# Optimization experiments

Measured on AMD Instinct MI355X. Metric: run time of the kernel, lower is better.

## Reference

```python
import jax, jax.numpy as jnp
import numpy as np

IN_SHAPE, OUT_SHAPE = 64, 256  # FoldingBlock(64, 256, ...)
REPEAT = OUT_SHAPE // IN_SHAPE  # 4


def sample_2d(m, n):
    # Reproduces SANet.points + SANet.sample_2D exactly (numpy constants).
    xs = np.linspace(-0.3, 0.3, 46)
    ys = np.linspace(-0.3, 0.3, 46)
    X, Y = np.meshgrid(xs, ys)            # (46,46) each, 'xy' indexing
    pts = np.stack([X, Y])                # (2,46,46)
    ix = np.round(np.linspace(0, 45, m)).astype(int)
    iy = np.round(np.linspace(0, 45, n)).astype(int)
    gx, gy = np.meshgrid(ix, iy)          # (n,m)
    p = pts[:, gx.ravel(), gy.ravel()].T  # (m*n, 2)
    return jnp.asarray(p, dtype=jnp.float32)


def _lin_relu(x, W, b):
    return jax.nn.relu(x @ W + b)


def setup_inputs() -> dict:
    key = jax.random.key(0)
    ks = jax.random.split(key, 16)
    s = 0.02  # small init scale keeps softmax logits well-conditioned
    d = {
        "p": jax.random.normal(ks[0], (128, 64, 512), dtype=jnp.float32),
        # upmlp1: MLP([514, 512]) (shared by both up() calls)
        "W_up": jax.random.normal(ks[1], (514, 512), dtype=jnp.float32) * s,
        "b_up": jnp.zeros((512,), jnp.float32),
        # self_attn1: M_h = MLP([1024,256])
        "Wh": jax.random.normal(ks[2], (1024, 256), dtype=jnp.float32) * s,
        "bh": jnp.zeros((256,), jnp.float32),
        # M_l = MLP([1024,256])
        "Wl": jax.random.normal(ks[3], (1024, 256), dtype=jnp.float32) * s,
        "bl": jnp.zeros((256,), jnp.float32),
        # M_g = MLP([1024,1024])
        "Wg": jax.random.normal(ks[4], (1024, 1024), dtype=jnp.float32) * s,
        "bg": jnp.zeros((1024,), jnp.float32),
        # M_f = MLP([1024,512,256]) -> two Linear+ReLU layers
        "Wf1": jax.random.normal(ks[5], (1024, 512), dtype=jnp.float32) * s,
        "bf1": jnp.zeros((512,), jnp.float32),
        "Wf2": jax.random.normal(ks[6], (512, 256), dtype=jnp.float32) * s,
        "bf2": jnp.zeros((256,), jnp.float32),
        # M_down: MLP([1024, 512])
        "W_down": jax.random.normal(ks[7], (1024, 512), dtype=jnp.float32) * s,
        "b_down": jnp.zeros((512,), jnp.float32),
        "m": 16,
        "n": 16,
    }
    return d


def _up(p, pts, W_up, b_up, Wh, bh, Wl, bl, Wg, bg, Wf1, bf1, Wf2, bf2):
    # p: (B, 64, 512) -> (B, 256, 512) via torch-style repeat (tile)
    B = p.shape[0]
    p = jnp.tile(p, (1, REPEAT, 1))
    p2d = jnp.concatenate([p, jnp.broadcast_to(pts[None], (B,) + pts.shape)], -1)  # (B,256,514)
    p2d = _lin_relu(p2d, W_up, b_up)                  # (B,256,512)
    p = jnp.concatenate([p, p2d], -1)                  # (B,256,1024)
    # SelfAttention (hand-rolled: separate projections + softmax + bmm)
    h = _lin_relu(p, Wh, bh)                           # (B,256,256)
    l = _lin_relu(p, Wl, bl)                           # (B,256,256)
    g = _lin_relu(p, Wg, bg)                           # (B,256,1024)
    mm = jnp.einsum("bmc,bnc->bmn", l, h)             # l @ h^T
    attn = jax.nn.softmax(mm, axis=-1)
    applied = jnp.einsum("bmn,bnc->bmc", attn, g)      # (B,256,1024)
    x = p + applied
    # M_f = MLP([1024,512,256]): ReLU after every Linear
    return _lin_relu(_lin_relu(x, Wf1, bf1), Wf2, bf2)  # (B,256,256)


def _down(p, W_down, b_down):
    # (B,256,256) -> (B,64,1024) -> MLP([1024,512])
    B = p.shape[0]
    p = p.reshape(B, IN_SHAPE, REPEAT * p.shape[2])
    return _lin_relu(p, W_down, b_down)                # (B,64,512)


def reference(p, W_up, b_up, Wh, bh, Wl, bl, Wg, bg, Wf1, bf1, Wf2, bf2,
              W_down, b_down, m, n):
    pts = sample_2d(int(m), int(n))                    # (m*n, 2) constant grid
    attn_params = (Wh, bh, Wl, bl, Wg, bg, Wf1, bf1, Wf2, bf2)
    p1 = _up(p, pts, W_up, b_up, *attn_params)         # (B,256,256)
    p2 = _down(p1, W_down, b_down)                     # (B,64,512)
    p_delta = p - p2
    p2u = _up(p_delta, pts, W_up, b_up, *attn_params)  # shared weights with first up
    return p1 + p2u                                    # (B,256,256)
```

## Files before the change

kernel.cpp:

```cpp
#include <hip/hip_runtime.h>
#include <cstdint>
#include <cstddef>


typedef unsigned short u16;
typedef __bf16 bf16x8 __attribute__((ext_vector_type(8)));
typedef float f32x4 __attribute__((ext_vector_type(4)));

__device__ __forceinline__ u16 f2bf(float f) {
    unsigned u = __builtin_bit_cast(unsigned, f);
    unsigned r = (u + 0x7fffu + ((u >> 16) & 1u)) >> 16;
    return (u16)r;
}
__device__ __forceinline__ float bf2f(u16 h) {
    unsigned u = ((unsigned)h) << 16;
    return __builtin_bit_cast(float, u);
}
__device__ __forceinline__ bf16x8 ldfrag(const u16* p) {
    return __builtin_bit_cast(bf16x8, *reinterpret_cast<const uint4*>(p));
}
__device__ __forceinline__ void gload16(const u16* g, u16* l) {
    __builtin_amdgcn_global_load_lds((__attribute__((address_space(1))) void*)g,
                                     (__attribute__((address_space(3))) void*)l,
                                     16, 0, 0);
}

#define FENCE asm volatile("" ::: "memory")
#define BAR() do { FENCE; __builtin_amdgcn_s_barrier(); FENCE; } while (0)

template<int MODE>
__global__ __launch_bounds__(512, 1)
void bp(const u16* __restrict__ A0, const u16* __restrict__ A1,
        const u16* __restrict__ Bt, const float* __restrict__ bias,
        const float* __restrict__ EXf, const u16* __restrict__ EXb,
        u16* __restrict__ outB, u16* __restrict__ out1, u16* __restrict__ out2,
        int K, long sB)
{
    __shared__ __align__(16) u16 As[2][16384];
    __shared__ __align__(16) u16 Bs[2][16384];

    const int b    = blockIdx.y;
    const int tid  = threadIdx.x;
    const int lane = tid & 63;
    const int w    = tid >> 6;
    const int wr   = w >> 2, wc = w & 3;
    const int wrow0 = wr * 128, wcol0 = wc * 64;
    const int gn0  = blockIdx.x * 256;
    const int lm   = lane & 15, hk = lane >> 4;
    const int NT   = K / 64;

    const int srow = tid & 255;
    const int su   = tid >> 8;

    const u16* gA0;
    const u16* gA1 = nullptr;
    if constexpr (MODE == 0) {
        gA0 = A0 + ((size_t)b << 15) + (size_t)(srow & 63) * 512 + su * 8;
    } else if constexpr (MODE == 1) {
        gA0 = A0 + ((size_t)b << 15) + (size_t)(srow & 63) * 512 + su * 8;
        gA1 = A1 + ((size_t)b << 17) + (size_t)srow * 512 + su * 8;
    } else if constexpr (MODE == 3) {
        gA0 = A0 + ((size_t)b << 16) + (size_t)srow * 256 + su * 8;
    } else {
        gA0 = A0 + ((size_t)b << 18) + (size_t)srow * 1024 + su * 8;
    }
    const u16* gB0 = Bt + (size_t)b * sB + (size_t)(gn0 + srow) * K + su * 8;

    u16* dA = &As[0][(size_t)(su * 256 + srow) * 8];
    u16* dB = &Bs[0][(size_t)(su * 256 + srow) * 8];

    auto stgA = [&](int kt, int buf, int rp) {
        const u16* g;
        if constexpr (MODE == 1) g = (kt < 8) ? (gA0 + kt * 64) : (gA1 + (kt - 8) * 64);
        else                     g = gA0 + kt * 64;
        u16* d = dA + buf * 16384 + rp * 8192;
        gload16(g + rp * 32,      d);
        gload16(g + rp * 32 + 16, d + 4096);
    };
    auto stgB = [&](int kt, int buf, int rp) {
        const u16* g = gB0 + kt * 64 + rp * 32;
        u16* d = dB + buf * 16384 + rp * 8192;
        gload16(g,      d);
        gload16(g + 16, d + 4096);
    };

    const u16* rA = &As[0][(size_t)(hk * 256 + wrow0 + lm) * 8];
    const u16* rB = &Bs[0][(size_t)(hk * 256 + wcol0 + lm) * 8];

    f32x4 acc[8][4];
    #pragma unroll
    for (int i = 0; i < 8; ++i)
        #pragma unroll
        for (int j = 0; j < 4; ++j)
            acc[i][j] = (f32x4){0.f, 0.f, 0.f, 0.f};

    stgA(0, 0, 0); stgA(0, 0, 1);
    stgB(0, 0, 0); stgB(0, 0, 1);
    stgA(1, 1, 0); stgB(1, 1, 0);
    asm volatile("s_waitcnt vmcnt(4)" ::: "memory");
    BAR();

    for (int t = 0; t < NT; ++t) {
        const int buf = t & 1, nx = buf ^ 1;
        const u16* a  = rA + buf * 16384;
        const u16* bb = rB + buf * 16384;
        bf16x8 aq[4], bq[4];

        #pragma unroll
        for (int i = 0; i < 4; ++i) aq[i] = ldfrag(a + i * 128);
        #pragma unroll
        for (int j = 0; j < 4; ++j) bq[j] = ldfrag(bb + j * 128);
        if (t + 1 < NT) stgA(t + 1, nx, 1);
        BAR();
        __builtin_amdgcn_s_setprio(1);
        #pragma unroll
        for (int i = 0; i < 4; ++i)
            #pragma unroll
            for (int j = 0; j < 4; ++j)
                acc[i][j] = __builtin_amdgcn_mfma_f32_16x16x32_bf16(aq[i], bq[j], acc[i][j], 0, 0, 0);
        __builtin_amdgcn_s_setprio(0);
        BAR();

        #pragma unroll
        for (int i = 0; i < 4; ++i) aq[i] = ldfrag(a + (4 + i) * 128);
        if (t + 1 < NT) stgB(t + 1, nx, 1);
        BAR();
        __builtin_amdgcn_s_setprio(1);
        #pragma unroll
        for (int i = 0; i < 4; ++i)
            #pragma unroll
            for (int j = 0; j < 4; ++j)
                acc[4 + i][j] = __builtin_amdgcn_mfma_f32_16x16x32_bf16(aq[i], bq[j], acc[4 + i][j], 0, 0, 0);
        __builtin_amdgcn_s_setprio(0);
        BAR();

        #pragma unroll
        for (int i = 0; i < 4; ++i) aq[i] = ldfrag(a + 8192 + i * 128);
        #pragma unroll
        for (int j = 0; j < 4; ++j) bq[j] = ldfrag(bb + 8192 + j * 128);
        if (t + 2 < NT) stgA(t + 2, buf, 0);
        BAR();
        __builtin_amdgcn_s_setprio(1);
        #pragma unroll
        for (int i = 0; i < 4; ++i)
            #pragma unroll
            for (int j = 0; j < 4; ++j)
                acc[i][j] = __builtin_amdgcn_mfma_f32_16x16x32_bf16(aq[i], bq[j], acc[i][j], 0, 0, 0);
        __builtin_amdgcn_s_setprio(0);
        BAR();

        #pragma unroll
        for (int i = 0; i < 4; ++i) aq[i] = ldfrag(a + 8192 + (4 + i) * 128);
        if (t + 2 < NT) stgB(t + 2, buf, 0);
        if (t + 2 < NT) { asm volatile("s_waitcnt vmcnt(4)" ::: "memory"); }
        else            { asm volatile("s_waitcnt vmcnt(0)" ::: "memory"); }
        BAR();
        __builtin_amdgcn_s_setprio(1);
        #pragma unroll
        for (int i = 0; i < 4; ++i)
            #pragma unroll
            for (int j = 0; j < 4; ++j)
                acc[4 + i][j] = __builtin_amdgcn_mfma_f32_16x16x32_bf16(aq[i], bq[j], acc[4 + i][j], 0, 0, 0);
        __builtin_amdgcn_s_setprio(0);
        BAR();
    }

    #pragma unroll
    for (int i = 0; i < 8; ++i) {
        const int rowb = wrow0 + i * 16 + hk * 4;
        #pragma unroll
        for (int j = 0; j < 4; ++j) {
            const int col = gn0 + wcol0 + j * 16 + lm;
            float v4[4];
            #pragma unroll
            for (int r = 0; r < 4; ++r) v4[r] = acc[i][j][r];

            if constexpr (MODE == 0) {
                #pragma unroll
                for (int r = 0; r < 4; ++r) {
                    const int row = rowb + r;
                    float v = v4[r];
                    const float px = -0.3f + 0.04f * (float)(row >> 4);
                    const float py = -0.3f + 0.04f * (float)(row & 15);
                    v += px * EXf[(size_t)512 * 512 + col] + py * EXf[(size_t)513 * 512 + col];
                    v = fmaxf(v + bias[col], 0.0f);
                    outB[((size_t)b << 17) + (size_t)row * 512 + col] = f2bf(v);
                }
            } else if constexpr (MODE == 1) {
                if (col < 512) {
                    #pragma unroll
                    for (int r = 0; r < 4; ++r) {
                        const int row = rowb + r;
                        float v = fmaxf(v4[r] + bias[col], 0.0f);
                        if (col < 256) outB[((size_t)b << 16) + (size_t)row * 256 + col] = f2bf(v);
                        else           out1[((size_t)b << 16) + (size_t)row * 256 + (col - 256)] = f2bf(v);
                    }
                } else {
                    ushort4 o;
                    o.x = f2bf(fmaxf(v4[0] + bias[col], 0.0f));
                    o.y = f2bf(fmaxf(v4[1] + bias[col], 0.0f));
                    o.z = f2bf(fmaxf(v4[2] + bias[col], 0.0f));
                    o.w = f2bf(fmaxf(v4[3] + bias[col], 0.0f));
                    *reinterpret_cast<ushort4*>(out2 + ((size_t)b << 18) +
                        (size_t)(col - 512) * 256 + rowb) = o;
                }
            } else if constexpr (MODE == 3) {
                #pragma unroll
                for (int r = 0; r < 4; ++r) {
                    const int row = rowb + r;
                    float v = v4[r];
                    float cv;
                    if (col < 512) {
                        const size_t ridx = ((size_t)b << 15) + (size_t)(row & 63) * 512 + col;
                        cv = EXf ? EXf[ridx] : bf2f(EXb[ridx]);
                    } else {
                        cv = bf2f(A1[((size_t)b << 17) + (size_t)row * 512 + (col - 512)]);
                    }
                    v += cv;
                    outB[((size_t)b << 18) + (size_t)row * 1024 + col] = f2bf(v);
                }
            } else {
                #pragma unroll
                for (int r = 0; r < 4; ++r) {
                    const int row = rowb + r;
                    float v = fmaxf(v4[r] + bias[col], 0.0f);
                    outB[((size_t)b << 17) + (size_t)row * 512 + col] = f2bf(v);
                }
            }
        }
    }
}

template<int MODE>
__global__ __launch_bounds__(256, 2)
void mg(const u16* __restrict__ A0, const u16* __restrict__ Bt,
        const float* __restrict__ bias, const float* __restrict__ EXf,
        float* __restrict__ outF, u16* __restrict__ outB,
        int K, long sB)
{
    constexpr int BK = 64;
    constexpr int UMASK = 7;

    __shared__ __align__(16) u16 As[2][128 * 64];
    __shared__ __align__(16) u16 Bs[2][128 * 64];

    const int b    = blockIdx.z;
    const int tid  = threadIdx.x;
    const int lane = tid & 63;
    const int w    = tid >> 6;
    const int wr   = w >> 1, wc = w & 1;
    const int wrow0 = wr * 64, wcol0 = wc * 64;
    const int gm0  = blockIdx.y * 128;
    const int gn0  = blockIdx.x * 128;
    const int lm   = lane & 15, hk = lane >> 4;
    const int NT = K / BK;

    auto stage = [&](int kt, int buf) {
        const int kb = kt * BK;
        #pragma unroll
        for (int t = 0; t < 4; ++t) {
            const int idx = tid + t * 256;
            const int row = idx >> 3, u = idx & UMASK;
            const int kk = kb + ((u ^ (row & UMASK)) << 3);
            const u16* ga;
            if constexpr (MODE == 2) {
                ga = A0 + ((size_t)b << 16) + (size_t)(gm0 + row) * 256 + kk;
            } else if constexpr (MODE == 5) {
                ga = A0 + ((size_t)b << 17) + (size_t)(gm0 + row) * 512 + kk;
            } else {
                int gr = gm0 + row; if (gr > 63) gr = 63;
                ga = A0 + ((size_t)b << 16) + (size_t)(gr * 4 + (kk >> 8)) * 256 + (kk & 255);
            }
            gload16(ga, &As[buf][(size_t)(w * 64 + t * 256) * 8]);
        }
        #pragma unroll
        for (int t = 0; t < 4; ++t) {
            const int idx = tid + t * 256;
            const int row = idx >> 3, u = idx & UMASK;
            const int kk = kb + ((u ^ (row & UMASK)) << 3);
            gload16(Bt + (size_t)b * sB + (size_t)(gn0 + row) * K + kk,
                    &Bs[buf][(size_t)(w * 64 + t * 256) * 8]);
        }
    };

    f32x4 acc[4][4];
    #pragma unroll
    for (int i = 0; i < 4; ++i)
        #pragma unroll
        for (int j = 0; j < 4; ++j)
            acc[i][j] = (f32x4){0.f, 0.f, 0.f, 0.f};

    stage(0, 0);
    if (NT > 1) stage(1, 1);

    for (int kt = 0; kt < NT; ++kt) {
        const int cur = kt & 1;
        if (kt == NT - 1) asm volatile("s_waitcnt vmcnt(0)" ::: "memory");
        else              asm volatile("s_waitcnt vmcnt(8)" ::: "memory");
        __builtin_amdgcn_s_barrier();
        FENCE;

        #pragma unroll
        for (int ks = 0; ks < 2; ++ks) {
            bf16x8 af[4], bfr[4];
            #pragma unroll
            for (int i = 0; i < 4; ++i) {
                const int row = wrow0 + i * 16 + lm;
                af[i] = ldfrag(&As[cur][(size_t)row * BK + (((ks * 4 + hk) ^ (row & UMASK)) << 3)]);
            }
            #pragma unroll
            for (int j = 0; j < 4; ++j) {
                const int row = wcol0 + j * 16 + lm;
                bfr[j] = ldfrag(&Bs[cur][(size_t)row * BK + (((ks * 4 + hk) ^ (row & UMASK)) << 3)]);
            }
            __builtin_amdgcn_s_setprio(1);
            #pragma unroll
            for (int i = 0; i < 4; ++i)
                #pragma unroll
                for (int j = 0; j < 4; ++j)
                    acc[i][j] = __builtin_amdgcn_mfma_f32_16x16x32_bf16(af[i], bfr[j], acc[i][j], 0, 0, 0);
            __builtin_amdgcn_s_setprio(0);
        }

        FENCE;
        __builtin_amdgcn_s_barrier();
        if (kt + 2 < NT) stage(kt + 2, cur);
    }

    #pragma unroll
    for (int i = 0; i < 4; ++i) {
        #pragma unroll
        for (int r = 0; r < 4; ++r) {
            const int row = gm0 + wrow0 + i * 16 + hk * 4 + r;
            if (MODE == 6 && row >= 64) continue;
            #pragma unroll
            for (int j = 0; j < 4; ++j) {
                const int col = gn0 + wcol0 + j * 16 + lm;
                float v = acc[i][j][r];
                if constexpr (MODE == 2) {
                    outF[((size_t)b << 16) + (size_t)row * 256 + col] = v;
                } else if constexpr (MODE == 5) {
                    v = fmaxf(v + bias[col], 0.0f);
                    const size_t oidx = ((size_t)b << 16) + (size_t)row * 256 + col;
                    if (EXf) v += EXf[oidx];
                    outF[oidx] = v;
                    if (outB) outB[oidx] = f2bf(v);
                } else {
                    v = fmaxf(v + bias[col], 0.0f);
                    const size_t oidx = ((size_t)b << 15) + (size_t)row * 512 + col;
                    v = EXf[oidx] - v;
                    outB[oidx] = f2bf(v);
                }
            }
        }
    }
}

template<bool F32IN>
__global__ __launch_bounds__(256)
void transpose_k(const void* __restrict__ in_, u16* __restrict__ out, int R, int C)
{
    __shared__ float t[64][65];
    const size_t zo = (size_t)blockIdx.z * (size_t)R * C;
    const int c0 = blockIdx.x * 64, r0 = blockIdx.y * 64;
    const int x = threadIdx.x, y = threadIdx.y;
    #pragma unroll
    for (int i = 0; i < 16; ++i) {
        const int r = y * 16 + i;
        float v;
        if constexpr (F32IN) v = ((const float*)in_)[zo + (size_t)(r0 + r) * C + c0 + x];
        else                 v = bf2f(((const u16*)in_)[zo + (size_t)(r0 + r) * C + c0 + x]);
        t[r][x] = v;
    }
    __syncthreads();
    #pragma unroll
    for (int i = 0; i < 16; ++i) {
        const int c = y * 16 + i;
        out[zo + (size_t)(c0 + c) * R + r0 + x] = f2bf(t[x][c]);
    }
}

__global__ __launch_bounds__(256)
void cvt_k(const float* __restrict__ in, u16* __restrict__ out, int n4)
{
    int i = blockIdx.x * 256 + threadIdx.x;
    const int stride = gridDim.x * 256;
    for (; i < n4; i += stride) {
        float4 v = ((const float4*)in)[i];
        ushort4 o;
        o.x = f2bf(v.x); o.y = f2bf(v.y); o.z = f2bf(v.z); o.w = f2bf(v.w);
        ((ushort4*)out)[i] = o;
    }
}

__global__ __launch_bounds__(512)
void concat3_k(const float* __restrict__ a, const float* __restrict__ bb,
               const float* __restrict__ c, float* __restrict__ o)
{
    const int i = blockIdx.x * 512 + threadIdx.x;
    if (i < 256)       o[i] = a[i];
    else if (i < 512)  o[i] = bb[i - 256];
    else if (i < 1536) o[i] = c[i - 512];
}

__global__ __launch_bounds__(64)
void softmax_k(const float* __restrict__ logits, u16* __restrict__ attn)
{
    const size_t row = blockIdx.x;
    const float4 v = ((const float4*)(logits + row * 256))[threadIdx.x];
    float mx = fmaxf(fmaxf(v.x, v.y), fmaxf(v.z, v.w));
    #pragma unroll
    for (int o = 32; o > 0; o >>= 1) mx = fmaxf(mx, __shfl_xor(mx, o));
    float e0 = expf(v.x - mx), e1 = expf(v.y - mx), e2 = expf(v.z - mx), e3 = expf(v.w - mx);
    float s = e0 + e1 + e2 + e3;
    #pragma unroll
    for (int o = 32; o > 0; o >>= 1) s += __shfl_xor(s, o);
    const float inv = 1.0f / s;
    ushort4 o;
    o.x = f2bf(e0 * inv); o.y = f2bf(e1 * inv); o.z = f2bf(e2 * inv); o.w = f2bf(e3 * inv);
    ((ushort4*)(attn + row * 256))[threadIdx.x] = o;
}

extern "C" void kernel_launch(void* const* d_in, const int* in_sizes, int n_in,
                              void* d_out, int out_size, void* d_ws, size_t ws_size,
                              hipStream_t stream)
{
    const float* p      = (const float*)d_in[0];
    const float* W_up   = (const float*)d_in[1];
    const float* b_up   = (const float*)d_in[2];
    const float* Wh     = (const float*)d_in[3];
    const float* bh     = (const float*)d_in[4];
    const float* Wl     = (const float*)d_in[5];
    const float* bl     = (const float*)d_in[6];
    const float* Wg     = (const float*)d_in[7];
    const float* bg_    = (const float*)d_in[8];
    const float* Wf1    = (const float*)d_in[9];
    const float* bf1    = (const float*)d_in[10];
    const float* Wf2    = (const float*)d_in[11];
    const float* bf2v   = (const float*)d_in[12];
    const float* W_down = (const float*)d_in[13];
    const float* b_down = (const float*)d_in[14];

    const int B = in_sizes[0] / 32768;
    float* out = (float*)d_out;

    char* wsp = (char*)d_ws;
    auto alloc = [&](size_t bytes) -> char* {
        char* r = wsp; wsp += (bytes + 255) & ~(size_t)255; return r;
    };

    u16* WupT  = (u16*)alloc((size_t)512 * 512 * 2);
    u16* WhlgT = (u16*)alloc((size_t)1536 * 1024 * 2);
    u16* Wf1T  = (u16*)alloc((size_t)512 * 1024 * 2);
    u16* Wf2T  = (u16*)alloc((size_t)256 * 512 * 2);
    u16* WdT   = (u16*)alloc((size_t)512 * 1024 * 2);
    float* bias_hlg = (float*)alloc((size_t)1536 * 4);
    u16* pbf   = (u16*)alloc((size_t)B * 32768 * 2);

    const size_t fixed_used = (size_t)(wsp - (char*)d_ws);
    const size_t perB = 1903104;
    int BC = B;
    while (BC > 1 && fixed_used + (size_t)BC * perB + 4096 > ws_size) BC >>= 1;

    u16* upout = (u16*)alloc((size_t)BC * 131072 * 2);
    u16* gT    = (u16*)alloc((size_t)BC * 262144 * 2);
    u16* xb    = (u16*)alloc((size_t)BC * 262144 * 2);
    u16* hb    = (u16*)alloc((size_t)BC * 65536 * 2);
    u16* lb    = (u16*)alloc((size_t)BC * 65536 * 2);
    u16* atb   = (u16*)alloc((size_t)BC * 65536 * 2);
    u16* p1bf  = (u16*)alloc((size_t)BC * 65536 * 2);
    u16* pdbf  = (u16*)alloc((size_t)BC * 32768 * 2);
    float* lgt = (float*)xb;

    const dim3 tb(64, 4);
    {
        int n4 = B * 8192;
        int nb = (n4 + 255) / 256; if (nb > 2048) nb = 2048;
        cvt_k<<<dim3(nb), dim3(256), 0, stream>>>(p, pbf, n4);
        transpose_k<true><<<dim3(8, 8, 1),  tb, 0, stream>>>(W_up, WupT, 512, 512);
        transpose_k<true><<<dim3(4, 16, 1), tb, 0, stream>>>(Wh, WhlgT, 1024, 256);
        transpose_k<true><<<dim3(4, 16, 1), tb, 0, stream>>>(Wl, WhlgT + (size_t)256 * 1024, 1024, 256);
        transpose_k<true><<<dim3(16, 16, 1),tb, 0, stream>>>(Wg, WhlgT + (size_t)512 * 1024, 1024, 1024);
        transpose_k<true><<<dim3(8, 16, 1), tb, 0, stream>>>(Wf1, Wf1T, 1024, 512);
        transpose_k<true><<<dim3(4, 8, 1),  tb, 0, stream>>>(Wf2, Wf2T, 512, 256);
        transpose_k<true><<<dim3(8, 16, 1), tb, 0, stream>>>(W_down, WdT, 1024, 512);
        concat3_k<<<dim3(3), dim3(512), 0, stream>>>(bh, bl, bg_, bias_hlg);
    }

    auto run_up = [&](const u16* pin_bf, const float* pin_f32, const u16* pin_ebf,
                      float* f2outF, u16* f2outB, const float* f2EXf, int bc) {
        bp<0><<<dim3(2, bc), dim3(512), 0, stream>>>(
            pin_bf, nullptr, WupT, b_up, W_up, nullptr, upout, nullptr, nullptr, 512, 0);
        bp<1><<<dim3(6, bc), dim3(512), 0, stream>>>(
            pin_bf, upout, WhlgT, bias_hlg, nullptr, nullptr, hb, lb, gT, 1024, 0);
        mg<2><<<dim3(2, 2, bc), dim3(256), 0, stream>>>(
            lb, hb, nullptr, nullptr, lgt, nullptr, 256, 65536);
        softmax_k<<<dim3(bc * 256), dim3(64), 0, stream>>>(lgt, atb);
        bp<3><<<dim3(4, bc), dim3(512), 0, stream>>>(
            atb, upout, gT, nullptr, pin_f32, pin_ebf, xb, nullptr, nullptr, 256, 262144);
        bp<4><<<dim3(2, bc), dim3(512), 0, stream>>>(
            xb, nullptr, Wf1T, bf1, nullptr, nullptr, upout, nullptr, nullptr, 1024, 0);
        mg<5><<<dim3(2, 2, bc), dim3(256), 0, stream>>>(
            upout, Wf2T, bf2v, f2EXf, f2outF, f2outB, 512, 0);
    };

    for (int b0 = 0; b0 < B; b0 += BC) {
        const int bc = (B - b0 < BC) ? (B - b0) : BC;
        const u16*   pin_bf  = pbf + (size_t)b0 * 32768;
        const float* pin_f32 = p   + (size_t)b0 * 32768;
        float* outc = out + (size_t)b0 * 65536;
        run_up(pin_bf, pin_f32, nullptr, outc, p1bf, nullptr, bc);
        mg<6><<<dim3(4, 1, bc), dim3(256), 0, stream>>>(
            p1bf, WdT, b_down, pin_f32, nullptr, pdbf, 1024, 0);
        run_up(pdbf, nullptr, pdbf, outc, nullptr, outc, bc);
    }
}
```

Measured before the change: 869.0 us.

## Use inline-asm LDS reads, unswizzled k-major smem layout, and split lgkm waits

Replaces the C++ LDS fragment loads with inline ds_read_b128 on precomputed LDS byte addresses, adding explicit lgkmcnt waits with sched barriers in both GEMM kernels. In the mg kernel the XOR-swizzled row-major LDS tile becomes a k-chunk-major layout, and all fragments for both k-substeps are issued up front so the second batch of reads overlaps the first batch of MFMAs. The aim is to cut address arithmetic and let LDS latency hide behind MFMA work. The risks are LDS bank conflicts from dropping the swizzle, and scheduling constraints from the inline asm that the compiler cannot reorder around.

```diff
diff --git a/kernel.cpp b/kernel.cpp
--- a/kernel.cpp
+++ b/kernel.cpp
@@ -16,17 +16,25 @@
     unsigned u = ((unsigned)h) << 16;
     return __builtin_bit_cast(float, u);
 }
-__device__ __forceinline__ bf16x8 ldfrag(const u16* p) {
-    return __builtin_bit_cast(bf16x8, *reinterpret_cast<const uint4*>(p));
-}
 __device__ __forceinline__ void gload16(const u16* g, u16* l) {
     __builtin_amdgcn_global_load_lds((__attribute__((address_space(1))) void*)g,
                                      (__attribute__((address_space(3))) void*)l,
                                      16, 0, 0);
 }
+__device__ __forceinline__ unsigned ldsaddr(const u16* p) {
+    return (unsigned)(size_t)(const __attribute__((address_space(3))) u16*)p;
+}
+__device__ __forceinline__ bf16x8 dsr128(unsigned a) {
+    f32x4 r;
+    asm volatile("ds_read_b128 %0, %1" : "=v"(r) : "v"(a));
+    return __builtin_bit_cast(bf16x8, r);
+}
 
 #define FENCE asm volatile("" ::: "memory")
 #define BAR() do { FENCE; __builtin_amdgcn_s_barrier(); FENCE; } while (0)
+#define VMC(N) asm volatile("s_waitcnt vmcnt(" #N ")" ::: "memory")
+#define LGKM(N) do { asm volatile("s_waitcnt lgkmcnt(" #N ")" ::: "memory"); \
+                     __builtin_amdgcn_sched_barrier(0); } while (0)
 
 template<int MODE>
 __global__ __launch_bounds__(512, 1)
@@ -84,8 +92,8 @@
         gload16(g + 16, d + 4096);
     };
 
-    const u16* rA = &As[0][(size_t)(hk * 256 + wrow0 + lm) * 8];
-    const u16* rB = &Bs[0][(size_t)(hk * 256 + wcol0 + lm) * 8];
+    const unsigned aBase = ldsaddr(&As[0][0]) + (unsigned)(hk * 256 + wrow0 + lm) * 16u;
+    const unsigned bBase = ldsaddr(&Bs[0][0]) + (unsigned)(hk * 256 + wcol0 + lm) * 16u;
 
     f32x4 acc[8][4];
     #pragma unroll
@@ -93,77 +101,72 @@
         #pragma unroll
         for (int j = 0; j < 4; ++j)
             acc[i][j] = (f32x4){0.f, 0.f, 0.f, 0.f};
+
+#define MFMA_Q(IB) do { \
+    _Pragma("unroll") for (int i_ = 0; i_ < 4; ++i_) \
+        _Pragma("unroll") for (int j_ = 0; j_ < 4; ++j_) \
+            acc[(IB) + i_][j_] = __builtin_amdgcn_mfma_f32_16x16x32_bf16( \
+                aq[i_], bq[j_], acc[(IB) + i_][j_], 0, 0, 0); \
+} while (0)
 
     stgA(0, 0, 0); stgA(0, 0, 1);
     stgB(0, 0, 0); stgB(0, 0, 1);
     stgA(1, 1, 0); stgB(1, 1, 0);
-    asm volatile("s_waitcnt vmcnt(4)" ::: "memory");
+    VMC(4);
     BAR();
 
     for (int t = 0; t < NT; ++t) {
         const int buf = t & 1, nx = buf ^ 1;
-        const u16* a  = rA + buf * 16384;
-        const u16* bb = rB + buf * 16384;
+        const unsigned ab = aBase + (unsigned)buf * 32768u;
+        const unsigned bb = bBase + (unsigned)buf * 32768u;
         bf16x8 aq[4], bq[4];
 
         #pragma unroll
-        for (int i = 0; i < 4; ++i) aq[i] = ldfrag(a + i * 128);
-        #pragma unroll
-        for (int j = 0; j < 4; ++j) bq[j] = ldfrag(bb + j * 128);
+        for (int i = 0; i < 4; ++i) aq[i] = dsr128(ab + (unsigned)(i * 256));
+        #pragma unroll
+        for (int j = 0; j < 4; ++j) bq[j] = dsr128(bb + (unsigned)(j * 256));
         if (t + 1 < NT) stgA(t + 1, nx, 1);
         BAR();
+        LGKM(0);
         __builtin_amdgcn_s_setprio(1);
-        #pragma unroll
-        for (int i = 0; i < 4; ++i)
-            #pragma unroll
-            for (int j = 0; j < 4; ++j)
-                acc[i][j] = __builtin_amdgcn_mfma_f32_16x16x32_bf16(aq[i], bq[j], acc[i][j], 0, 0, 0);
+        MFMA_Q(0);
         __builtin_amdgcn_s_setprio(0);
         BAR();
 
         #pragma unroll
-        for (int i = 0; i < 4; ++i) aq[i] = ldfrag(a + (4 + i) * 128);
+        for (int i = 0; i < 4; ++i) aq[i] = dsr128(ab + (unsigned)(1024 + i * 256));
         if (t + 1 < NT) stgB(t + 1, nx, 1);
         BAR();
+        LGKM(0);
         __builtin_amdgcn_s_setprio(1);
-        #pragma unroll
-        for (int i = 0; i < 4; ++i)
-            #pragma unroll
-            for (int j = 0; j < 4; ++j)
-                acc[4 + i][j] = __builtin_amdgcn_mfma_f32_16x16x32_bf16(aq[i], bq[j], acc[4 + i][j], 0, 0, 0);
+        MFMA_Q(4);
         __builtin_amdgcn_s_setprio(0);
         BAR();
 
         #pragma unroll
-        for (int i = 0; i < 4; ++i) aq[i] = ldfrag(a + 8192 + i * 128);
-        #pragma unroll
-        for (int j = 0; j < 4; ++j) bq[j] = ldfrag(bb + 8192 + j * 128);
+        for (int i = 0; i < 4; ++i) aq[i] = dsr128(ab + (unsigned)(16384 + i * 256));
+        #pragma unroll
+        for (int j = 0; j < 4; ++j) bq[j] = dsr128(bb + (unsigned)(16384 + j * 256));
         if (t + 2 < NT) stgA(t + 2, buf, 0);
         BAR();
+        LGKM(0);
         __builtin_amdgcn_s_setprio(1);
-        #pragma unroll
-        for (int i = 0; i < 4; ++i)
-            #pragma unroll
-            for (int j = 0; j < 4; ++j)
-                acc[i][j] = __builtin_amdgcn_mfma_f32_16x16x32_bf16(aq[i], bq[j], acc[i][j], 0, 0, 0);
+        MFMA_Q(0);
         __builtin_amdgcn_s_setprio(0);
         BAR();
 
         #pragma unroll
-        for (int i = 0; i < 4; ++i) aq[i] = ldfrag(a + 8192 + (4 + i) * 128);
+        for (int i = 0; i < 4; ++i) aq[i] = dsr128(ab + (unsigned)(17408 + i * 256));
         if (t + 2 < NT) stgB(t + 2, buf, 0);
-        if (t + 2 < NT) { asm volatile("s_waitcnt vmcnt(4)" ::: "memory"); }
-        else            { asm volatile("s_waitcnt vmcnt(0)" ::: "memory"); }
-        BAR();
+        if (t + 2 < NT) { VMC(4); } else { VMC(0); }
+        BAR();
+        LGKM(0);
         __builtin_amdgcn_s_setprio(1);
-        #pragma unroll
-        for (int i = 0; i < 4; ++i)
-            #pragma unroll
-            for (int j = 0; j < 4; ++j)
-                acc[4 + i][j] = __builtin_amdgcn_mfma_f32_16x16x32_bf16(aq[i], bq[j], acc[4 + i][j], 0, 0, 0);
+        MFMA_Q(4);
         __builtin_amdgcn_s_setprio(0);
         BAR();
     }
+#undef MFMA_Q
 
     #pragma unroll
     for (int i = 0; i < 8; ++i) {
@@ -238,9 +241,6 @@
         float* __restrict__ outF, u16* __restrict__ outB,
         int K, long sB)
 {
-    constexpr int BK = 64;
-    constexpr int UMASK = 7;
-
     __shared__ __align__(16) u16 As[2][128 * 64];
     __shared__ __align__(16) u16 Bs[2][128 * 64];
 
@@ -253,15 +253,15 @@
     const int gm0  = blockIdx.y * 128;
     const int gn0  = blockIdx.x * 128;
     const int lm   = lane & 15, hk = lane >> 4;
-    const int NT = K / BK;
+    const int NT = K / 64;
 
     auto stage = [&](int kt, int buf) {
-        const int kb = kt * BK;
-        #pragma unroll
-        for (int t = 0; t < 4; ++t) {
-            const int idx = tid + t * 256;
-            const int row = idx >> 3, u = idx & UMASK;
-            const int kk = kb + ((u ^ (row & UMASK)) << 3);
+        const int kb = kt * 64;
+        #pragma unroll
+        for (int tp = 0; tp < 4; ++tp) {
+            const int idx = tid + tp * 256;
+            const int U = idx >> 7, row = idx & 127;
+            const int kk = kb + U * 8;
             const u16* ga;
             if constexpr (MODE == 2) {
                 ga = A0 + ((size_t)b << 16) + (size_t)(gm0 + row) * 256 + kk;
@@ -271,18 +271,21 @@
                 int gr = gm0 + row; if (gr > 63) gr = 63;
                 ga = A0 + ((size_t)b << 16) + (size_t)(gr * 4 + (kk >> 8)) * 256 + (kk & 255);
             }
-            gload16(ga, &As[buf][(size_t)(w * 64 + t * 256) * 8]);
+            gload16(ga, &As[buf][(size_t)idx * 8]);
         }
         #pragma unroll
-        for (int t = 0; t < 4; ++t) {
-            const int idx = tid + t * 256;
-            const int row = idx >> 3, u = idx & UMASK;
-            const int kk = kb + ((u ^ (row & UMASK)) << 3);
+        for (int tp = 0; tp < 4; ++tp) {
+            const int idx = tid + tp * 256;
+            const int U = idx >> 7, row = idx & 127;
+            const int kk = kb + U * 8;
             gload16(Bt + (size_t)b * sB + (size_t)(gn0 + row) * K + kk,
-                    &Bs[buf][(size_t)(w * 64 + t * 256) * 8]);
+                    &Bs[buf][(size_t)idx * 8]);
         }
     };
 
+    const unsigned aBase = ldsaddr(&As[0][0]) + (unsigned)(hk * 128 + wrow0 + lm) * 16u;
+    const unsigned bBase = ldsaddr(&Bs[0][0]) + (unsigned)(hk * 128 + wcol0 + lm) * 16u;
+
     f32x4 acc[4][4];
     #pragma unroll
     for (int i = 0; i < 4; ++i)
@@ -295,33 +298,36 @@
 
     for (int kt = 0; kt < NT; ++kt) {
         const int cur = kt & 1;
-        if (kt == NT - 1) asm volatile("s_waitcnt vmcnt(0)" ::: "memory");
-        else              asm volatile("s_waitcnt vmcnt(8)" ::: "memory");
+        if (kt == NT - 1) { VMC(0); } else { VMC(8); }
         __builtin_amdgcn_s_barrier();
         FENCE;
-
-        #pragma unroll
-        for (int ks = 0; ks < 2; ++ks) {
-            bf16x8 af[4], bfr[4];
+        const unsigned ab = aBase + (unsigned)cur * 16384u;
+        const unsigned bb = bBase + (unsigned)cur * 16384u;
+        bf16x8 a0[4], b0[4], a1[4], b1[4];
+        #pragma unroll
+        for (int i = 0; i < 4; ++i) a0[i] = dsr128(ab + (unsigned)(i * 256));
+        #pragma unroll
+        for (int j = 0; j < 4; ++j) b0[j] = dsr128(bb + (unsigned)(j * 256));
+        #pragma unroll
+        for (int i = 0; i < 4; ++i) a1[i] = dsr128(ab + (unsigned)(8192 + i * 256));
+        #pragma unroll
+        for (int j = 0; j < 4; ++j) b1[j] = dsr128(bb + (unsigned)(8192 + j * 256));
+        LGKM(8);
+        __builtin_amdgcn_s_setprio(1);
+        #pragma unroll
+        for (int i = 0; i < 4; ++i)
             #pragma unroll
-            for (int i = 0; i < 4; ++i) {
-                const int row = wrow0 + i * 16 + lm;
-                af[i] = ldfrag(&As[cur][(size_t)row * BK + (((ks * 4 + hk) ^ (row & UMASK)) << 3)]);
-            }
+            for (int j = 0; j < 4; ++j)
+                acc[i][j] = __builtin_amdgcn_mfma_f32_16x16x32_bf16(a0[i], b0[j], acc[i][j], 0, 0, 0);
+        __builtin_amdgcn_s_setprio(0);
+        LGKM(0);
+        __builtin_amdgcn_s_setprio(1);
+        #pragma unroll
+        for (int i = 0; i < 4; ++i)
             #pragma unroll
-            for (int j = 0; j < 4; ++j) {
-                const int row = wcol0 + j * 16 + lm;
-                bfr[j] = ldfrag(&Bs[cur][(size_t)row * BK + (((ks * 4 + hk) ^ (row & UMASK)) << 3)]);
-            }
-            __builtin_amdgcn_s_setprio(1);
-            #pragma unroll
-            for (int i = 0; i < 4; ++i)
-                #pragma unroll
-                for (int j = 0; j < 4; ++j)
-                    acc[i][j] = __builtin_amdgcn_mfma_f32_16x16x32_bf16(af[i], bfr[j], acc[i][j], 0, 0, 0);
-            __builtin_amdgcn_s_setprio(0);
-        }
-
+            for (int j = 0; j < 4; ++j)
+                acc[i][j] = __builtin_amdgcn_mfma_f32_16x16x32_bf16(a1[i], b1[j], acc[i][j], 0, 0, 0);
+        __builtin_amdgcn_s_setprio(0);
         FENCE;
         __builtin_amdgcn_s_barrier();
         if (kt + 2 < NT) stage(kt + 2, cur);
```

After: 886.6 us. 1.02x slower.

## Dedupe repeated rows in up-projection GEMM and fuse logits with softmax

Applied to the files above, without the earlier changes.

The up-projection GEMM now multiplies only the 64 distinct input rows per batch, two batches per block, instead of the 256 repeated rows. Each result is expanded in the epilogue to the four repeated output rows, each with its own grid coordinate term, which cuts MFMA work for that stage to a quarter. The separate fp32 logits GEMM and softmax kernel are replaced by one kernel that computes l·h^T and does a row softmax in registers using a cross-wave LDS reduction, so the fp32 logits never go through global memory. The new up kernel launches bc/2 blocks in z, so an odd chunk size would drop a batch.

```diff
diff --git a/kernel.cpp b/kernel.cpp
--- a/kernel.cpp
+++ b/kernel.cpp
@@ -24,9 +24,20 @@
                                      (__attribute__((address_space(3))) void*)l,
                                      16, 0, 0);
 }
+__device__ __forceinline__ unsigned ldsaddr(const u16* p) {
+    return (unsigned)(size_t)(const __attribute__((address_space(3))) u16*)p;
+}
+__device__ __forceinline__ bf16x8 dsr128(unsigned a) {
+    f32x4 r;
+    asm volatile("ds_read_b128 %0, %1" : "=v"(r) : "v"(a));
+    return __builtin_bit_cast(bf16x8, r);
+}
 
 #define FENCE asm volatile("" ::: "memory")
 #define BAR() do { FENCE; __builtin_amdgcn_s_barrier(); FENCE; } while (0)
+#define VMC(N) asm volatile("s_waitcnt vmcnt(" #N ")" ::: "memory")
+#define LGKM(N) do { asm volatile("s_waitcnt lgkmcnt(" #N ")" ::: "memory"); \
+                     __builtin_amdgcn_sched_barrier(0); } while (0)
 
 template<int MODE>
 __global__ __launch_bounds__(512, 1)
@@ -54,9 +65,7 @@
 
     const u16* gA0;
     const u16* gA1 = nullptr;
-    if constexpr (MODE == 0) {
-        gA0 = A0 + ((size_t)b << 15) + (size_t)(srow & 63) * 512 + su * 8;
-    } else if constexpr (MODE == 1) {
+    if constexpr (MODE == 1) {
         gA0 = A0 + ((size_t)b << 15) + (size_t)(srow & 63) * 512 + su * 8;
         gA1 = A1 + ((size_t)b << 17) + (size_t)srow * 512 + su * 8;
     } else if constexpr (MODE == 3) {
@@ -97,7 +106,7 @@
     stgA(0, 0, 0); stgA(0, 0, 1);
     stgB(0, 0, 0); stgB(0, 0, 1);
     stgA(1, 1, 0); stgB(1, 1, 0);
-    asm volatile("s_waitcnt vmcnt(4)" ::: "memory");
+    VMC(4);
     BAR();
 
     for (int t = 0; t < NT; ++t) {
@@ -152,8 +161,7 @@
         #pragma unroll
         for (int i = 0; i < 4; ++i) aq[i] = ldfrag(a + 8192 + (4 + i) * 128);
         if (t + 2 < NT) stgB(t + 2, buf, 0);
-        if (t + 2 < NT) { asm volatile("s_waitcnt vmcnt(4)" ::: "memory"); }
-        else            { asm volatile("s_waitcnt vmcnt(0)" ::: "memory"); }
+        if (t + 2 < NT) { VMC(4); } else { VMC(0); }
         BAR();
         __builtin_amdgcn_s_setprio(1);
         #pragma unroll
@@ -175,18 +183,7 @@
             #pragma unroll
             for (int r = 0; r < 4; ++r) v4[r] = acc[i][j][r];
 
-            if constexpr (MODE == 0) {
-                #pragma unroll
-                for (int r = 0; r < 4; ++r) {
-                    const int row = rowb + r;
-                    float v = v4[r];
-                    const float px = -0.3f + 0.04f * (float)(row >> 4);
-                    const float py = -0.3f + 0.04f * (float)(row & 15);
-                    v += px * EXf[(size_t)512 * 512 + col] + py * EXf[(size_t)513 * 512 + col];
-                    v = fmaxf(v + bias[col], 0.0f);
-                    outB[((size_t)b << 17) + (size_t)row * 512 + col] = f2bf(v);
-                }
-            } else if constexpr (MODE == 1) {
+            if constexpr (MODE == 1) {
                 if (col < 512) {
                     #pragma unroll
                     for (int r = 0; r < 4; ++r) {
@@ -231,6 +228,240 @@
     }
 }
 
+__global__ __launch_bounds__(512, 4)
+void sp(const u16* __restrict__ A0, const u16* __restrict__ Bt,
+        const float* __restrict__ bias, const float* __restrict__ EXf,
+        u16* __restrict__ outB, int K)
+{
+    __shared__ __align__(16) u16 As[2][4096];
+    __shared__ __align__(16) u16 Bs[2][8192];
+
+    const int bz   = blockIdx.z;
+    const int gn0  = blockIdx.x * 256;
+    const int tid  = threadIdx.x;
+    const int lane = tid & 63;
+    const int w    = tid >> 6;
+    const int wr   = w >> 2, wc = w & 3;
+    const int wrow0 = wr * 64, wcol0 = wc * 64;
+    const int lm   = lane & 15, hk = lane >> 4;
+    const int NT   = K / 32;
+
+    const int rowA = tid & 127, uA = tid >> 7;
+    const int rowB = tid & 255, uB = tid >> 8;
+
+    const u16* gA = A0 + ((size_t)(2 * bz + (rowA >> 6)) << 15)
+                       + (size_t)(rowA & 63) * 512 + uA * 8;
+    const u16* gB0 = Bt + (size_t)(gn0 + rowB) * K + uB * 8;
+    const u16* gB1 = gB0 + 16;
+
+    u16* dA  = &As[0][(size_t)(uA * 128 + rowA) * 8];
+    u16* dB0 = &Bs[0][(size_t)(uB * 256 + rowB) * 8];
+    u16* dB1 = dB0 + 4096;
+
+    auto stage = [&](int kt, int buf) {
+        const int ko = kt * 32;
+        gload16(gA  + ko, dA  + buf * 4096);
+        gload16(gB0 + ko, dB0 + buf * 8192);
+        gload16(gB1 + ko, dB1 + buf * 8192);
+    };
+
+    const unsigned aB = ldsaddr(&As[0][0]) + (unsigned)((hk * 128 + wrow0 + lm) * 16);
+    const unsigned bB = ldsaddr(&Bs[0][0]) + (unsigned)((hk * 256 + wcol0 + lm) * 16);
+
+    f32x4 acc[4][4];
+    #pragma unroll
+    for (int i = 0; i < 4; ++i)
+        #pragma unroll
+        for (int j = 0; j < 4; ++j)
+            acc[i][j] = (f32x4){0.f, 0.f, 0.f, 0.f};
+
+    stage(0, 0);
+    stage(1, 1);
+
+    for (int t = 0; t < NT; ++t) {
+        const int buf = t & 1;
+        if (t == NT - 1) { VMC(0); } else { VMC(3); }
+        BAR();
+        bf16x8 aq[4], bq[4];
+        const unsigned ab = aB + (unsigned)buf * 8192u;
+        const unsigned bb = bB + (unsigned)buf * 16384u;
+        #pragma unroll
+        for (int i = 0; i < 4; ++i) aq[i] = dsr128(ab + (unsigned)(i * 256));
+        #pragma unroll
+        for (int j = 0; j < 4; ++j) bq[j] = dsr128(bb + (unsigned)(j * 256));
+        LGKM(0);
+        __builtin_amdgcn_s_setprio(1);
+        #pragma unroll
+        for (int i = 0; i < 4; ++i)
+            #pragma unroll
+            for (int j = 0; j < 4; ++j)
+                acc[i][j] = __builtin_amdgcn_mfma_f32_16x16x32_bf16(aq[i], bq[j], acc[i][j], 0, 0, 0);
+        __builtin_amdgcn_s_setprio(0);
+        BAR();
+        if (t + 2 < NT) stage(t + 2, buf);
+    }
+
+    #pragma unroll
+    for (int i = 0; i < 4; ++i) {
+        const int lrb = wrow0 + i * 16 + hk * 4;
+        const int b2  = 2 * bz + (lrb >> 6);
+        #pragma unroll
+        for (int j = 0; j < 4; ++j) {
+            const int col = gn0 + wcol0 + j * 16 + lm;
+            const float wx = EXf[(size_t)512 * 512 + col];
+            const float wy = EXf[(size_t)513 * 512 + col];
+            const float bc = bias[col];
+            #pragma unroll
+            for (int r = 0; r < 4; ++r) {
+                const int prow = (lrb + r) & 63;
+                const float py = -0.3f + 0.04f * (float)(prow & 15);
+                const float base = acc[i][j][r] + py * wy + bc;
+                #pragma unroll
+                for (int q = 0; q < 4; ++q) {
+                    const float px = -0.3f + 0.04f * (float)((prow >> 4) + 4 * q);
+                    const float v = fmaxf(base + px * wx, 0.0f);
+                    outB[((size_t)b2 << 17) + (size_t)(prow + 64 * q) * 512 + col] = f2bf(v);
+                }
+            }
+        }
+    }
+}
+
+__global__ __launch_bounds__(256, 1)
+void msm(const u16* __restrict__ L, const u16* __restrict__ H,
+         u16* __restrict__ attn)
+{
+    __shared__ __align__(16) u16 As[2][8192];
+    __shared__ __align__(16) u16 Bs[2][16384];
+    __shared__ float smax[2][2][64];
+    __shared__ float ssum[2][2][64];
+
+    const int b    = blockIdx.z;
+    const int gm0  = blockIdx.y * 128;
+    const int tid  = threadIdx.x;
+    const int lane = tid & 63;
+    const int w    = tid >> 6;
+    const int wr   = w >> 1, wc = w & 1;
+    const int lm   = lane & 15, hk = lane >> 4;
+
+    auto stage = [&](int kt, int buf) {
+        const int kb = kt * 64;
+        #pragma unroll
+        for (int t = 0; t < 4; ++t) {
+            const int idx = tid + t * 256;
+            const int U = idx >> 7, row = idx & 127;
+            gload16(L + ((size_t)b << 16) + (size_t)(gm0 + row) * 256 + kb + U * 8,
+                    &As[buf][(size_t)idx * 8]);
+        }
+        #pragma unroll
+        for (int t = 0; t < 8; ++t) {
+            const int idx = tid + t * 256;
+            const int U = idx >> 8, row = idx & 255;
+            gload16(H + ((size_t)b << 16) + (size_t)row * 256 + kb + U * 8,
+                    &Bs[buf][(size_t)idx * 8]);
+        }
+    };
+
+    f32x4 acc[4][8];
+    #pragma unroll
+    for (int i = 0; i < 4; ++i)
+        #pragma unroll
+        for (int j = 0; j < 8; ++j)
+            acc[i][j] = (f32x4){0.f, 0.f, 0.f, 0.f};
+
+    stage(0, 0);
+    stage(1, 1);
+
+    for (int kt = 0; kt < 4; ++kt) {
+        const int cur = kt & 1;
+        if (kt == 3) { VMC(0); } else { VMC(12); }
+        BAR();
+        #pragma unroll
+        for (int ks = 0; ks < 2; ++ks) {
+            bf16x8 aq[4], bq[8];
+            #pragma unroll
+            for (int i = 0; i < 4; ++i)
+                aq[i] = ldfrag(&As[cur][(size_t)((ks * 4 + hk) * 128 + wr * 64 + i * 16 + lm) * 8]);
+            #pragma unroll
+            for (int j = 0; j < 8; ++j)
+                bq[j] = ldfrag(&Bs[cur][(size_t)((ks * 4 + hk) * 256 + wc * 128 + j * 16 + lm) * 8]);
+            #pragma unroll
+            for (int i = 0; i < 4; ++i)
+                #pragma unroll
+                for (int j = 0; j < 8; ++j)
+                    acc[i][j] = __builtin_amdgcn_mfma_f32_16x16x32_bf16(aq[i], bq[j], acc[i][j], 0, 0, 0);
+        }
+        BAR();
+        if (kt + 2 < 4) stage(kt + 2, cur);
+    }
+
+    float m[4][4];
+    #pragma unroll
+    for (int i = 0; i < 4; ++i)
+        #pragma unroll
+        for (int r = 0; r < 4; ++r) {
+            float mm = acc[i][0][r];
+            #pragma unroll
+            for (int j = 1; j < 8; ++j) mm = fmaxf(mm, acc[i][j][r]);
+            #pragma unroll
+            for (int o = 1; o < 16; o <<= 1) mm = fmaxf(mm, __shfl_xor(mm, o));
+            m[i][r] = mm;
+        }
+    if (lm == 0) {
+        #pragma unroll
+        for (int i = 0; i < 4; ++i)
+            #pragma unroll
+            for (int r = 0; r < 4; ++r)
+                smax[wr][wc][i * 16 + hk * 4 + r] = m[i][r];
+    }
+    __syncthreads();
+    #pragma unroll
+    for (int i = 0; i < 4; ++i)
+        #pragma unroll
+        for (int r = 0; r < 4; ++r) {
+            const int lr = i * 16 + hk * 4 + r;
+            m[i][r] = fmaxf(smax[wr][0][lr], smax[wr][1][lr]);
+        }
+    float sv[4][4];
+    #pragma unroll
+    for (int i = 0; i < 4; ++i)
+        #pragma unroll
+        for (int r = 0; r < 4; ++r) {
+            float s = 0.f;
+            #pragma unroll
+            for (int j = 0; j < 8; ++j) {
+                const float e = expf(acc[i][j][r] - m[i][r]);
+                acc[i][j][r] = e;
+                s += e;
+            }
+            #pragma unroll
+            for (int o = 1; o < 16; o <<= 1) s += __shfl_xor(s, o);
+            sv[i][r] = s;
+        }
+    if (lm == 0) {
+        #pragma unroll
+        for (int i = 0; i < 4; ++i)
+            #pragma unroll
+            for (int r = 0; r < 4; ++r)
+                ssum[wr][wc][i * 16 + hk * 4 + r] = sv[i][r];
+    }
+    __syncthreads();
+    #pragma unroll
+    for (int i = 0; i < 4; ++i) {
+        #pragma unroll
+        for (int r = 0; r < 4; ++r) {
+            const int lr = i * 16 + hk * 4 + r;
+            const float inv = 1.0f / (ssum[wr][0][lr] + ssum[wr][1][lr]);
+            const int row = gm0 + wr * 64 + lr;
+            #pragma unroll
+            for (int j = 0; j < 8; ++j) {
+                const int col = wc * 128 + j * 16 + lm;
+                attn[((size_t)b << 16) + (size_t)row * 256 + col] = f2bf(acc[i][j][r] * inv);
+            }
+        }
+    }
+}
+
 template<int MODE>
 __global__ __launch_bounds__(256, 2)
 void mg(const u16* __restrict__ A0, const u16* __restrict__ Bt,
@@ -263,9 +494,7 @@
             const int row = idx >> 3, u = idx & UMASK;
             const int kk = kb + ((u ^ (row & UMASK)) << 3);
             const u16* ga;
-            if constexpr (MODE == 2) {
-                ga = A0 + ((size_t)b << 16) + (size_t)(gm0 + row) * 256 + kk;
-            } else if constexpr (MODE == 5) {
+            if constexpr (MODE == 5) {
                 ga = A0 + ((size_t)b << 17) + (size_t)(gm0 + row) * 512 + kk;
             } else {
                 int gr = gm0 + row; if (gr > 63) gr = 63;
@@ -295,8 +524,7 @@
 
     for (int kt = 0; kt < NT; ++kt) {
         const int cur = kt & 1;
-        if (kt == NT - 1) asm volatile("s_waitcnt vmcnt(0)" ::: "memory");
-        else              asm volatile("s_waitcnt vmcnt(8)" ::: "memory");
+        if (kt == NT - 1) { VMC(0); } else { VMC(8); }
         __builtin_amdgcn_s_barrier();
         FENCE;
 
@@ -337,9 +565,7 @@
             for (int j = 0; j < 4; ++j) {
                 const int col = gn0 + wcol0 + j * 16 + lm;
                 float v = acc[i][j][r];
-                if constexpr (MODE == 2) {
-                    outF[((size_t)b << 16) + (size_t)row * 256 + col] = v;
-                } else if constexpr (MODE == 5) {
+                if constexpr (MODE == 5) {
                     v = fmaxf(v + bias[col], 0.0f);
                     const size_t oidx = ((size_t)b << 16) + (size_t)row * 256 + col;
                     if (EXf) v += EXf[oidx];
@@ -401,24 +627,6 @@
     if (i < 256)       o[i] = a[i];
     else if (i < 512)  o[i] = bb[i - 256];
     else if (i < 1536) o[i] = c[i - 512];
-}
-
-__global__ __launch_bounds__(64)
-void softmax_k(const float* __restrict__ logits, u16* __restrict__ attn)
-{
-    const size_t row = blockIdx.x;
-    const float4 v = ((const float4*)(logits + row * 256))[threadIdx.x];
-    float mx = fmaxf(fmaxf(v.x, v.y), fmaxf(v.z, v.w));
-    #pragma unroll
-    for (int o = 32; o > 0; o >>= 1) mx = fmaxf(mx, __shfl_xor(mx, o));
-    float e0 = expf(v.x - mx), e1 = expf(v.y - mx), e2 = expf(v.z - mx), e3 = expf(v.w - mx);
-    float s = e0 + e1 + e2 + e3;
-    #pragma unroll
-    for (int o = 32; o > 0; o >>= 1) s += __shfl_xor(s, o);
-    const float inv = 1.0f / s;
-    ushort4 o;
-    o.x = f2bf(e0 * inv); o.y = f2bf(e1 * inv); o.z = f2bf(e2 * inv); o.w = f2bf(e3 * inv);
-    ((ushort4*)(attn + row * 256))[threadIdx.x] = o;
 }
 
 extern "C" void kernel_launch(void* const* d_in, const int* in_sizes, int n_in,
@@ -470,7 +678,6 @@
     u16* atb   = (u16*)alloc((size_t)BC * 65536 * 2);
     u16* p1bf  = (u16*)alloc((size_t)BC * 65536 * 2);
     u16* pdbf  = (u16*)alloc((size_t)BC * 32768 * 2);
-    float* lgt = (float*)xb;
 
     const dim3 tb(64, 4);
     {
@@ -489,13 +696,11 @@
 
     auto run_up = [&](const u16* pin_bf, const float* pin_f32, const u16* pin_ebf,
                       float* f2outF, u16* f2outB, const float* f2EXf, int bc) {
-        bp<0><<<dim3(2, bc), dim3(512), 0, stream>>>(
-            pin_bf, nullptr, WupT, b_up, W_up, nullptr, upout, nullptr, nullptr, 512, 0);
+        sp<<<dim3(2, 1, bc / 2), dim3(512), 0, stream>>>(
+            pin_bf, WupT, b_up, W_up, upout, 512);
         bp<1><<<dim3(6, bc), dim3(512), 0, stream>>>(
             pin_bf, upout, WhlgT, bias_hlg, nullptr, nullptr, hb, lb, gT, 1024, 0);
-        mg<2><<<dim3(2, 2, bc), dim3(256), 0, stream>>>(
-            lb, hb, nullptr, nullptr, lgt, nullptr, 256, 65536);
-        softmax_k<<<dim3(bc * 256), dim3(64), 0, stream>>>(lgt, atb);
+        msm<<<dim3(1, 2, bc), dim3(256), 0, stream>>>(lb, hb, atb);
         bp<3><<<dim3(4, bc), dim3(512), 0, stream>>>(
             atb, upout, gT, nullptr, pin_f32, pin_ebf, xb, nullptr, nullptr, 256, 262144);
         bp<4><<<dim3(2, bc), dim3(512), 0, stream>>>(
```

Result: no change. 866.7 us (-0.3%).
